# Kernel tuning notes

Measured on AMD Instinct MI355X. Metric: run time of the kernel, lower is better.

Reference implementation:

```python
import math
import jax, jax.numpy as jnp
import numpy as np

B, N, C, HEADS, EXTRA = 16, 577, 768, 12, 1
IMG = (24, 24)
LAMBDA = 0.6


def make_rel_index():
    Hh, Ww = IMG
    coords = np.stack(np.meshgrid(np.arange(Hh), np.arange(Ww), indexing='ij')).reshape(2, -1)
    rel = (coords[:, :, None] - coords[:, None, :]).transpose(1, 2, 0).astype(np.int64)
    rel[..., 0] += Hh - 1
    rel[..., 1] += Ww - 1
    rel[..., 0] *= 2 * Ww - 1
    idx = rel.sum(-1)
    idx = np.pad(idx, ((EXTRA, 0), (EXTRA, 0)))  # pad extra-token rows/cols with index 0
    return jnp.asarray(idx, dtype=jnp.int32)


def setup_inputs() -> dict:
    key = jax.random.key(0)
    ks = jax.random.split(key, 4)
    x = jax.random.normal(ks[0], (B, N, C), jnp.float32)
    qkv_w = jax.random.normal(ks[1], (3 * C, C), jnp.float32) * 0.02
    proj_w = jax.random.normal(ks[2], (C, C), jnp.float32) * 0.02
    proj_b = jnp.zeros((C,), jnp.float32)
    table_sz = (2 * IMG[0] - 1) * (2 * IMG[1] - 1) + 1  # 2210
    bias_table = jax.random.normal(ks[3], (table_sz, HEADS), jnp.float32) * 0.02
    token_weights = jnp.array([0.5, 0.5], jnp.float32)  # softmax([.5,.5]) at init
    return {"x": x, "qkv_w": qkv_w, "proj_w": proj_w, "proj_b": proj_b,
            "bias_table": bias_table, "token_weights": token_weights,
            "rel_index": make_rel_index()}


def attention(x, qkv_w, proj_w, proj_b, bias_table, rel_index):
    b, n, c = x.shape
    hd = c // HEADS
    scale = hd ** -0.5
    qkv = (x @ qkv_w.T).reshape(b, n, 3, HEADS, hd).transpose(2, 0, 3, 1, 4)
    q, k, v = qkv[0] * scale, qkv[1], qkv[2]  # (b,H,n,hd)
    attn = jnp.einsum('bhnd,bhmd->bhnm', q, k)
    bias = jnp.transpose(bias_table[rel_index], (2, 0, 1))  # (H,N,N)
    attn = jax.nn.softmax(attn + bias[None], axis=-1)
    out = jnp.einsum('bhnm,bhmd->bhnd', attn, v).transpose(0, 2, 1, 3).reshape(b, n, c)
    return out @ proj_w.T + proj_b, attn


def select_indices(attn, token_weights):
    # eager, data-dependent sizing (mirrors torch .tolist()/set() host logic)
    n = N - EXTRA
    cls_attn = attn[:, :, 0, EXTRA:].mean(axis=1)  # (B, n)
    avg = cls_attn.mean(axis=1, keepdims=True)
    mx = cls_attn.max(axis=1, keepdims=True)
    counts = np.asarray(((cls_attn >= avg) & (cls_attn <= mx)).sum(axis=1))
    T = counts.sum() / counts.shape[0]
    sig = 1.0 / (1.0 + math.exp(-(float(counts.max()) - float(T)) / B))
    keep = int(round(n * (LAMBDA + (1.0 - LAMBDA) * sig)))
    avg_extra = attn[:, :, :EXTRA, EXTRA:].mean(axis=1)  # (B, EXTRA, n)
    all_idx = []
    for e in range(EXTRA):
        ti = jax.lax.top_k(avg_extra[:, e, :], keep)[1]
        all_idx.extend(np.asarray(ti).reshape(-1).tolist())
    keep_idx = np.array(list(dict.fromkeys(all_idx))[:keep], dtype=np.int32)
    remaining = N - (EXTRA + keep)
    w = jax.nn.softmax(token_weights)
    num_text = int(float(w[0]) * remaining)
    num_img = remaining - num_text
    kt, ki = jax.random.split(jax.random.key(1))
    text_idx = jax.random.randint(kt, (B, max(num_text, 0)), 0, EXTRA)
    img_idx = jax.random.randint(ki, (B, max(num_img, 0)), 0, n - EXTRA)
    return jnp.asarray(keep_idx), text_idx, img_idx


def assemble(x_out, y, keep_idx, text_idx, img_idx):
    b, _, c = x_out.shape
    x_sel = x_out[:, EXTRA:][:, keep_idx]  # shared indices across batch
    parts = [x_out[:, :EXTRA], x_sel]
    if text_idx.shape[1] > 0:
        text_tokens = y[:, 1:1 + EXTRA]
        gi = jnp.broadcast_to(text_idx[:, :, None], (b, text_idx.shape[1], c))
        parts.append(jnp.take_along_axis(text_tokens, gi, axis=1))
    if img_idx.shape[1] > 0:
        image_tokens = y[:, 1 + EXTRA:]
        gi = jnp.broadcast_to(img_idx[:, :, None], (b, img_idx.shape[1], c))
        parts.append(jnp.take_along_axis(image_tokens, gi, axis=1))
    return jnp.concatenate(parts, axis=1)


def reference(x, qkv_w, proj_w, proj_b, bias_table, token_weights, rel_index):
    out, attn = attention(x, qkv_w, proj_w, proj_b, bias_table, rel_index)
    keep_idx, text_idx, img_idx = select_indices(attn, token_weights)
    return assemble(out, x, keep_idx, text_idx, img_idx)
```

## Files before the change

kernel.cpp:

```cpp
#include <hip/hip_runtime.h>
#include <math.h>

#define B_    16
#define N_    577
#define C_    768
#define H_    12
#define HD_   64
#define M_    (B_ * N_)
#define QKV_N 2304
#define NIMG  576

typedef _Float16 half8  __attribute__((ext_vector_type(8)));
typedef _Float16 half4v __attribute__((ext_vector_type(4)));
typedef float    floatx4 __attribute__((ext_vector_type(4)));

#define OFF_QKV      0u
#define OFF_ATTNH    21270528u
#define OFF_ATTNL    24815616u
#define OFF_XOUT     28360704u
#define OFF_CLS      35450880u
#define OFF_CLSPART  35460096u
#define OFF_META     35570688u
#define OFF_WQKVH    35580544u
#define OFF_WQKVL    36465280u
#define OFF_WPROJH   37350016u
#define OFF_WPROJL   37644928u
#define OFF_BIASEXP  37939840u

__global__ __launch_bounds__(256) void split_kernel(const float* __restrict__ in,
                                                    _Float16* __restrict__ hi,
                                                    _Float16* __restrict__ lo, int n) {
    int i = (blockIdx.x * 256 + threadIdx.x) * 4;
    if (i >= n) return;
    float4 v = *(const float4*)(in + i);
    half4v h, l;
    float vv[4] = {v.x, v.y, v.z, v.w};
#pragma unroll
    for (int j = 0; j < 4; ++j) {
        _Float16 hj = (_Float16)vv[j];
        h[j] = hj;
        l[j] = (_Float16)(vv[j] - (float)hj);
    }
    *(half4v*)(hi + i) = h;
    *(half4v*)(lo + i) = l;
}

__global__ __launch_bounds__(256) void bias_expand(const float* __restrict__ bias_table,
                                                   const int* __restrict__ rel_index,
                                                   _Float16* __restrict__ bias_exp) {
    int i = blockIdx.x, h = blockIdx.y;
    const int* ri = rel_index + (size_t)i * N_;
    _Float16* dst = bias_exp + ((size_t)h * N_ + i) * N_;
    for (int j = threadIdx.x; j < N_; j += 256)
        dst[j] = (_Float16)bias_table[ri[j] * H_ + h];
}

__global__ __launch_bounds__(256) void hgemm_nt_split(const _Float16* __restrict__ Ah,
                                                      const _Float16* __restrict__ Al,
                                                      const _Float16* __restrict__ Bh,
                                                      const _Float16* __restrict__ Bl,
                                                      const float* __restrict__ bias,
                                                      float* __restrict__ Cout,
                                                      int M, int Nout) {
    const int K = 768;
    __shared__ __attribute__((aligned(16))) _Float16 Ah_s[128][40];
    __shared__ __attribute__((aligned(16))) _Float16 Al_s[128][40];
    __shared__ __attribute__((aligned(16))) _Float16 Bh_s[128][40];
    __shared__ __attribute__((aligned(16))) _Float16 Bl_s[128][40];

    int tid = threadIdx.x;
    int wave = tid >> 6, lane = tid & 63;
    int g = lane >> 4, c = lane & 15;
    int wr = wave >> 1, wc = wave & 1;
    int m0 = blockIdx.y * 128, n0 = blockIdx.x * 128;

    floatx4 acc[4][4];
#pragma unroll
    for (int mi = 0; mi < 4; ++mi)
#pragma unroll
        for (int ni = 0; ni < 4; ++ni) { acc[mi][ni][0] = 0.f; acc[mi][ni][1] = 0.f; acc[mi][ni][2] = 0.f; acc[mi][ni][3] = 0.f; }

    int lr = tid >> 2;
    int lc = (tid & 3) << 3;

    for (int k0 = 0; k0 < K; k0 += 32) {
        __syncthreads();
#pragma unroll
        for (int hh = 0; hh < 2; ++hh) {
            int r2 = lr + hh * 64;
            size_t ga = (size_t)(m0 + r2) * K + k0 + lc;
            size_t gb = (size_t)(n0 + r2) * K + k0 + lc;
            *(half8*)&Ah_s[r2][lc] = *(const half8*)(Ah + ga);
            *(half8*)&Al_s[r2][lc] = *(const half8*)(Al + ga);
            *(half8*)&Bh_s[r2][lc] = *(const half8*)(Bh + gb);
            *(half8*)&Bl_s[r2][lc] = *(const half8*)(Bl + gb);
        }
        __syncthreads();

        half8 af_h[4], af_l[4];
#pragma unroll
        for (int mi = 0; mi < 4; ++mi) {
            af_h[mi] = *(const half8*)&Ah_s[wr * 64 + mi * 16 + c][g * 8];
            af_l[mi] = *(const half8*)&Al_s[wr * 64 + mi * 16 + c][g * 8];
        }
#pragma unroll
        for (int ni = 0; ni < 4; ++ni) {
            half8 bf_h = *(const half8*)&Bh_s[wc * 64 + ni * 16 + c][g * 8];
            half8 bf_l = *(const half8*)&Bl_s[wc * 64 + ni * 16 + c][g * 8];
#pragma unroll
            for (int mi = 0; mi < 4; ++mi) {
                acc[mi][ni] = __builtin_amdgcn_mfma_f32_16x16x32_f16(af_h[mi], bf_h, acc[mi][ni], 0, 0, 0);
                acc[mi][ni] = __builtin_amdgcn_mfma_f32_16x16x32_f16(af_h[mi], bf_l, acc[mi][ni], 0, 0, 0);
                acc[mi][ni] = __builtin_amdgcn_mfma_f32_16x16x32_f16(af_l[mi], bf_h, acc[mi][ni], 0, 0, 0);
            }
        }
    }

#pragma unroll
    for (int ni = 0; ni < 4; ++ni) {
        int col = n0 + wc * 64 + ni * 16 + c;
        float bv = bias ? bias[col] : 0.f;
#pragma unroll
        for (int mi = 0; mi < 4; ++mi) {
#pragma unroll
            for (int r = 0; r < 4; ++r) {
                int row = m0 + wr * 64 + mi * 16 + 4 * g + r;
                if (row < M) Cout[(size_t)row * Nout + col] = acc[mi][ni][r] + bv;
            }
        }
    }
}

__global__ __launch_bounds__(256, 2) void attn_mfma(const float* __restrict__ qkv,
                                                    const _Float16* __restrict__ bias_exp,
                                                    _Float16* __restrict__ attnh,
                                                    _Float16* __restrict__ attnl) {
    __shared__ __attribute__((aligned(16))) _Float16 Kh[64][72];
    __shared__ __attribute__((aligned(16))) _Float16 Kl[64][72];
    __shared__ __attribute__((aligned(16))) _Float16 Vh[64][72];
    __shared__ __attribute__((aligned(16))) _Float16 Vl[64][72];
    __shared__ __attribute__((aligned(16))) _Float16 Pb[4][32][72];

    int bh = blockIdx.y;
    int b = bh / H_, h = bh % H_;
    int tid = threadIdx.x;
    int wave = tid >> 6, lane = tid & 63;
    int g = lane >> 4, c = lane & 15;
    int row0 = blockIdx.x * 128 + wave * 32;

    half8 qh[2][2], ql[2][2];
#pragma unroll
    for (int rt = 0; rt < 2; ++rt) {
        int grow = row0 + rt * 16 + c;
#pragma unroll
        for (int kb = 0; kb < 2; ++kb) {
            floatx4 a0 = {0.f, 0.f, 0.f, 0.f}, a1 = {0.f, 0.f, 0.f, 0.f};
            if (grow < N_) {
                const float* src = qkv + (size_t)(b * N_ + grow) * QKV_N + h * HD_ + kb * 32 + g * 8;
                a0 = *(const floatx4*)src;
                a1 = *(const floatx4*)(src + 4);
            }
#pragma unroll
            for (int i = 0; i < 4; ++i) {
                float x0 = a0[i] * 0.125f;
                float x1 = a1[i] * 0.125f;
                _Float16 h0 = (_Float16)x0, h1 = (_Float16)x1;
                qh[rt][kb][i]     = h0; ql[rt][kb][i]     = (_Float16)(x0 - (float)h0);
                qh[rt][kb][i + 4] = h1; ql[rt][kb][i + 4] = (_Float16)(x1 - (float)h1);
            }
        }
    }

    floatx4 o[2][4];
    float mrun[2][4], lrun[2][4];
#pragma unroll
    for (int rt = 0; rt < 2; ++rt) {
#pragma unroll
        for (int t = 0; t < 4; ++t) { o[rt][t][0] = 0.f; o[rt][t][1] = 0.f; o[rt][t][2] = 0.f; o[rt][t][3] = 0.f; }
#pragma unroll
        for (int r = 0; r < 4; ++r) { mrun[rt][r] = -1e30f; lrun[rt][r] = 0.f; }
    }

    for (int j0 = 0; j0 < N_; j0 += 64) {
        __syncthreads();
#pragma unroll
        for (int it = 0; it < 4; ++it) {
            int p = tid + it * 256;
            int kr = p >> 4;
            int c4 = (p & 15) << 2;
            int key = j0 + kr;
            floatx4 kv = {0.f, 0.f, 0.f, 0.f}, vv = {0.f, 0.f, 0.f, 0.f};
            if (key < N_) {
                const float* base = qkv + (size_t)(b * N_ + key) * QKV_N + h * HD_ + c4;
                kv = *(const floatx4*)(base + 768);
                vv = *(const floatx4*)(base + 1536);
            }
            half4v kh_, kl_;
#pragma unroll
            for (int i = 0; i < 4; ++i) {
                _Float16 hi = (_Float16)kv[i];
                kh_[i] = hi; kl_[i] = (_Float16)(kv[i] - (float)hi);
            }
            *(half4v*)&Kh[kr][c4] = kh_;
            *(half4v*)&Kl[kr][c4] = kl_;
#pragma unroll
            for (int i = 0; i < 4; ++i) {
                _Float16 hi = (_Float16)vv[i];
                Vh[c4 + i][kr] = hi;
                Vl[c4 + i][kr] = (_Float16)(vv[i] - (float)hi);
            }
        }
        __syncthreads();

        float bv[2][4][4];
#pragma unroll
        for (int rt = 0; rt < 2; ++rt)
#pragma unroll
            for (int t = 0; t < 4; ++t)
#pragma unroll
                for (int r = 0; r < 4; ++r) {
                    int row = row0 + rt * 16 + 4 * g + r;
                    int key = j0 + t * 16 + c;
                    int rr = row < N_ ? row : N_ - 1;
                    int kk = key < N_ ? key : N_ - 1;
                    float bb = (float)bias_exp[((size_t)h * N_ + rr) * N_ + kk];
                    bv[rt][t][r] = (row < N_ && key < N_) ? bb : -1e30f;
                }

        floatx4 s[2][4];
#pragma unroll
        for (int rt = 0; rt < 2; ++rt)
#pragma unroll
            for (int t = 0; t < 4; ++t) { s[rt][t][0] = 0.f; s[rt][t][1] = 0.f; s[rt][t][2] = 0.f; s[rt][t][3] = 0.f; }
#pragma unroll
        for (int t = 0; t < 4; ++t) {
#pragma unroll
            for (int kb = 0; kb < 2; ++kb) {
                half8 kh8 = *(const half8*)&Kh[t * 16 + c][kb * 32 + g * 8];
                half8 kl8 = *(const half8*)&Kl[t * 16 + c][kb * 32 + g * 8];
#pragma unroll
                for (int rt = 0; rt < 2; ++rt) {
                    s[rt][t] = __builtin_amdgcn_mfma_f32_16x16x32_f16(qh[rt][kb], kh8, s[rt][t], 0, 0, 0);
                    s[rt][t] = __builtin_amdgcn_mfma_f32_16x16x32_f16(qh[rt][kb], kl8, s[rt][t], 0, 0, 0);
                    s[rt][t] = __builtin_amdgcn_mfma_f32_16x16x32_f16(ql[rt][kb], kh8, s[rt][t], 0, 0, 0);
                }
            }
        }

#pragma unroll
        for (int rt = 0; rt < 2; ++rt) {
#pragma unroll
            for (int t = 0; t < 4; ++t)
#pragma unroll
                for (int r = 0; r < 4; ++r) s[rt][t][r] += bv[rt][t][r];
            float pm[4], mnew[4], corr[4], rs[4];
#pragma unroll
            for (int r = 0; r < 4; ++r) {
                pm[r] = fmaxf(fmaxf(s[rt][0][r], s[rt][1][r]), fmaxf(s[rt][2][r], s[rt][3][r]));
            }
#pragma unroll
            for (int r = 0; r < 4; ++r) {
                pm[r] = fmaxf(pm[r], __shfl_xor(pm[r], 1));
                pm[r] = fmaxf(pm[r], __shfl_xor(pm[r], 2));
                pm[r] = fmaxf(pm[r], __shfl_xor(pm[r], 4));
                pm[r] = fmaxf(pm[r], __shfl_xor(pm[r], 8));
                mnew[r] = fmaxf(mrun[rt][r], pm[r]);
                corr[r] = __expf(mrun[rt][r] - mnew[r]);
                rs[r] = 0.f;
            }
#pragma unroll
            for (int t = 0; t < 4; ++t)
#pragma unroll
                for (int r = 0; r < 4; ++r) {
                    float p = __expf(s[rt][t][r] - mnew[r]);
                    s[rt][t][r] = p;
                    rs[r] += p;
                }
#pragma unroll
            for (int r = 0; r < 4; ++r) {
                rs[r] += __shfl_xor(rs[r], 1);
                rs[r] += __shfl_xor(rs[r], 2);
                rs[r] += __shfl_xor(rs[r], 4);
                rs[r] += __shfl_xor(rs[r], 8);
                lrun[rt][r] = lrun[rt][r] * corr[r] + rs[r];
                mrun[rt][r] = mnew[r];
            }
#pragma unroll
            for (int t = 0; t < 4; ++t)
#pragma unroll
                for (int r = 0; r < 4; ++r) o[rt][t][r] *= corr[r];
#pragma unroll
            for (int t = 0; t < 4; ++t)
#pragma unroll
                for (int r = 0; r < 4; ++r)
                    Pb[wave][rt * 16 + 4 * g + r][t * 16 + c] = (_Float16)s[rt][t][r];
        }

#pragma unroll
        for (int kb = 0; kb < 2; ++kb) {
            half8 pa[2];
#pragma unroll
            for (int rt = 0; rt < 2; ++rt)
                pa[rt] = *(const half8*)&Pb[wave][rt * 16 + c][kb * 32 + g * 8];
#pragma unroll
            for (int t = 0; t < 4; ++t) {
                half8 vh8 = *(const half8*)&Vh[t * 16 + c][kb * 32 + g * 8];
                half8 vl8 = *(const half8*)&Vl[t * 16 + c][kb * 32 + g * 8];
#pragma unroll
                for (int rt = 0; rt < 2; ++rt) {
                    o[rt][t] = __builtin_amdgcn_mfma_f32_16x16x32_f16(pa[rt], vh8, o[rt][t], 0, 0, 0);
                    o[rt][t] = __builtin_amdgcn_mfma_f32_16x16x32_f16(pa[rt], vl8, o[rt][t], 0, 0, 0);
                }
            }
        }
    }

#pragma unroll
    for (int rt = 0; rt < 2; ++rt)
#pragma unroll
        for (int t = 0; t < 4; ++t)
#pragma unroll
            for (int r = 0; r < 4; ++r) {
                int row = row0 + rt * 16 + 4 * g + r;
                if (row < N_) {
                    float val = o[rt][t][r] / lrun[rt][r];
                    size_t idx = (size_t)(b * N_ + row) * C_ + h * HD_ + t * 16 + c;
                    _Float16 hi = (_Float16)val;
                    attnh[idx] = hi;
                    attnl[idx] = (_Float16)(val - (float)hi);
                }
            }
}

__global__ __launch_bounds__(256) void cls_head_kernel(const float* __restrict__ qkv,
                                                       const float* __restrict__ bias_table,
                                                       const int* __restrict__ rel_index,
                                                       float* __restrict__ cls_part) {
    int b = blockIdx.x, h = blockIdx.y;
    __shared__ float q0[64];
    __shared__ float s[N_];
    __shared__ float red[256];
    int tid = threadIdx.x;
    if (tid < 64) q0[tid] = qkv[(size_t)(b * N_) * QKV_N + h * HD_ + tid] * 0.125f;
    __syncthreads();
    for (int j = tid; j < N_; j += 256) {
        const float* kr = qkv + (size_t)(b * N_ + j) * QKV_N + 768 + h * HD_;
        float d = 0.f;
        for (int kk = 0; kk < 64; ++kk) d += q0[kk] * kr[kk];
        s[j] = d + bias_table[rel_index[j] * H_ + h];
    }
    __syncthreads();
    float mx = -1e30f;
    for (int j = tid; j < N_; j += 256) mx = fmaxf(mx, s[j]);
    red[tid] = mx;
    __syncthreads();
    for (int st = 128; st > 0; st >>= 1) {
        if (tid < st) red[tid] = fmaxf(red[tid], red[tid + st]);
        __syncthreads();
    }
    float m = red[0];
    __syncthreads();
    float ssum = 0.f;
    for (int j = tid; j < N_; j += 256) ssum += expf(s[j] - m);
    red[tid] = ssum;
    __syncthreads();
    for (int st = 128; st > 0; st >>= 1) {
        if (tid < st) red[tid] += red[tid + st];
        __syncthreads();
    }
    float tot = red[0];
    __syncthreads();
    float* dst = cls_part + (size_t)(b * H_ + h) * NIMG;
    for (int j = tid; j < NIMG; j += 256) dst[j] = expf(s[j + 1] - m) / tot;
}

__global__ __launch_bounds__(576) void cls_reduce_kernel(const float* __restrict__ cls_part,
                                                         float* __restrict__ cls) {
    int b = blockIdx.x;
    int j = threadIdx.x;
    float a = 0.f;
    for (int h = 0; h < H_; ++h) a += cls_part[(size_t)(b * H_ + h) * NIMG + j];
    cls[b * NIMG + j] = a * (1.0f / 12.0f);
}

__device__ __forceinline__ void tf2x32(unsigned k0, unsigned k1, unsigned x0, unsigned x1,
                                       unsigned& o0, unsigned& o1) {
    unsigned ks2 = k0 ^ k1 ^ 0x1BD11BDAu;
    x0 += k0; x1 += k1;
#define ROTL_(v, d) (((v) << (d)) | ((v) >> (32 - (d))))
#define RND_(d) { x0 += x1; x1 = ROTL_(x1, d); x1 ^= x0; }
    RND_(13) RND_(15) RND_(26) RND_(6)
    x0 += k1; x1 += ks2 + 1u;
    RND_(17) RND_(29) RND_(16) RND_(24)
    x0 += ks2; x1 += k0 + 2u;
    RND_(13) RND_(15) RND_(26) RND_(6)
    x0 += k0; x1 += k1 + 3u;
    RND_(17) RND_(29) RND_(16) RND_(24)
    x0 += k1; x1 += ks2 + 4u;
    RND_(13) RND_(15) RND_(26) RND_(6)
    x0 += ks2; x1 += k0 + 5u;
    o0 = x0; o1 = x1;
#undef RND_
#undef ROTL_
}

__global__ __launch_bounds__(256) void select_kernel(const float* __restrict__ cls,
                                                     const float* __restrict__ token_w,
                                                     int* __restrict__ meta,
                                                     int* __restrict__ keep_idx,
                                                     int* __restrict__ img_idx) {
    __shared__ float red[256];
    __shared__ int ired[256];
    __shared__ int counts[16];
    __shared__ float c0[NIMG];
    __shared__ int keep_sh, nimg_sh;
    int tid = threadIdx.x;

    for (int b = 0; b < 16; ++b) {
        float sm = 0.f;
        for (int j = tid; j < NIMG; j += 256) sm += cls[b * NIMG + j];
        red[tid] = sm;
        __syncthreads();
        for (int st = 128; st > 0; st >>= 1) {
            if (tid < st) red[tid] += red[tid + st];
            __syncthreads();
        }
        float avg = red[0] * (1.0f / 576.0f);
        __syncthreads();
        int cnt = 0;
        for (int j = tid; j < NIMG; j += 256) cnt += (cls[b * NIMG + j] >= avg) ? 1 : 0;
        ired[tid] = cnt;
        __syncthreads();
        for (int st = 128; st > 0; st >>= 1) {
            if (tid < st) ired[tid] += ired[tid + st];
            __syncthreads();
        }
        if (tid == 0) counts[b] = ired[0];
        __syncthreads();
    }

    if (tid == 0) {
        int csum = 0, cmax = 0;
        for (int b2 = 0; b2 < 16; ++b2) {
            csum += counts[b2];
            if (counts[b2] > cmax) cmax = counts[b2];
        }
        double T = (double)csum / 16.0;
        double sig = 1.0 / (1.0 + exp(-(((double)cmax) - T) / 16.0));
        double kd = 576.0 * (0.6 + 0.4 * sig);
        int keep = (int)llrint(kd);
        int remaining = NIMG - keep;
        float w0 = token_w[0], w1 = token_w[1];
        float wm = fmaxf(w0, w1);
        float e0 = expf(w0 - wm), e1 = expf(w1 - wm);
        float wsm = e0 / (e0 + e1);
        int ntext = (int)((double)wsm * (double)remaining);
        int nimg = remaining - ntext;
        meta[0] = keep; meta[1] = ntext; meta[2] = nimg;
        keep_sh = keep; nimg_sh = nimg;
    }
    __syncthreads();

    for (int j = tid; j < NIMG; j += 256) c0[j] = cls[j];
    __syncthreads();
    int keep = keep_sh;
    for (int j = tid; j < NIMG; j += 256) {
        float v = c0[j];
        int rank = 0;
        for (int j2 = 0; j2 < NIMG; ++j2) {
            float v2 = c0[j2];
            rank += ((v2 > v) || (v2 == v && j2 < j)) ? 1 : 0;
        }
        if (rank < keep) keep_idx[rank] = j;
    }

    unsigned ki0, ki1, k1a, k1b, k2a, k2b;
    tf2x32(0u, 1u, 0u, 1u, ki0, ki1);
    tf2x32(ki0, ki1, 0u, 0u, k1a, k1b);
    tf2x32(ki0, ki1, 0u, 1u, k2a, k2b);
    int nimg = nimg_sh;
    int S = 16 * nimg;
    const unsigned span = 575u;
    const unsigned mult = ((65536u % span) * (65536u % span)) % span;
    for (int i = tid; i < S; i += 256) {
        unsigned h0, h1, l0, l1;
        tf2x32(k1a, k1b, 0u, (unsigned)i, h0, h1);
        tf2x32(k2a, k2b, 0u, (unsigned)i, l0, l1);
        unsigned hb = h0 ^ h1;
        unsigned lb = l0 ^ l1;
        unsigned off = ((hb % span) * mult + (lb % span)) % span;
        img_idx[i] = (int)off;
    }
}

__global__ __launch_bounds__(192) void assemble_kernel(const float* __restrict__ xout,
                                                       const float* __restrict__ x,
                                                       const int* __restrict__ meta,
                                                       const int* __restrict__ keep_idx,
                                                       const int* __restrict__ img_idx,
                                                       float* __restrict__ out) {
    int gb = blockIdx.x;
    int token = gb % N_;
    int b = gb / N_;
    int keep = meta[0], ntext = meta[1], nimg = meta[2];
    const float* src;
    if (token == 0) {
        src = xout + (size_t)(b * N_) * C_;
    } else if (token <= keep) {
        src = xout + (size_t)(b * N_ + 1 + keep_idx[token - 1]) * C_;
    } else if (token <= keep + ntext) {
        src = x + (size_t)(b * N_ + 1) * C_;
    } else {
        int t = token - 1 - keep - ntext;
        src = x + (size_t)(b * N_ + 2 + img_idx[b * nimg + t]) * C_;
    }
    float4* d = (float4*)(out + (size_t)(b * N_ + token) * C_);
    d[threadIdx.x] = ((const float4*)src)[threadIdx.x];
}

extern "C" void kernel_launch(void* const* d_in, const int* in_sizes, int n_in,
                              void* d_out, int out_size, void* d_ws, size_t ws_size,
                              hipStream_t stream) {
    const float* x          = (const float*)d_in[0];
    const float* qkv_w      = (const float*)d_in[1];
    const float* proj_w     = (const float*)d_in[2];
    const float* proj_b     = (const float*)d_in[3];
    const float* bias_table = (const float*)d_in[4];
    const float* token_w    = (const float*)d_in[5];
    const int*   rel_index  = (const int*)d_in[6];
    float* out = (float*)d_out;
    float* ws  = (float*)d_ws;

    float*     qkv_buf  = ws + OFF_QKV;
    _Float16*  attnh    = (_Float16*)(ws + OFF_ATTNH);
    _Float16*  attnl    = (_Float16*)(ws + OFF_ATTNL);
    float*     xout     = ws + OFF_XOUT;
    _Float16*  xh       = (_Float16*)(ws + OFF_XOUT);
    _Float16*  xl       = (_Float16*)(ws + OFF_XOUT + 3545088u);
    float*     cls      = ws + OFF_CLS;
    float*     cls_part = ws + OFF_CLSPART;
    int*       meta     = (int*)(ws + OFF_META);
    int*       keep_idx = meta + 8;
    int*       img_idx  = keep_idx + 576;
    _Float16*  wqkvh    = (_Float16*)(ws + OFF_WQKVH);
    _Float16*  wqkvl    = (_Float16*)(ws + OFF_WQKVL);
    _Float16*  wprojh   = (_Float16*)(ws + OFF_WPROJH);
    _Float16*  wprojl   = (_Float16*)(ws + OFF_WPROJL);
    _Float16*  bias_exp = (_Float16*)(ws + OFF_BIASEXP);

    split_kernel<<<dim3(M_ * C_ / 1024), 256, 0, stream>>>(x, xh, xl, M_ * C_);
    split_kernel<<<dim3(QKV_N * C_ / 1024), 256, 0, stream>>>(qkv_w, wqkvh, wqkvl, QKV_N * C_);
    split_kernel<<<dim3(C_ * C_ / 1024), 256, 0, stream>>>(proj_w, wprojh, wprojl, C_ * C_);
    bias_expand<<<dim3(N_, H_), 256, 0, stream>>>(bias_table, rel_index, bias_exp);
    hgemm_nt_split<<<dim3(QKV_N / 128, (M_ + 127) / 128), 256, 0, stream>>>(
        xh, xl, wqkvh, wqkvl, nullptr, qkv_buf, M_, QKV_N);
    cls_head_kernel<<<dim3(B_, H_), 256, 0, stream>>>(qkv_buf, bias_table, rel_index, cls_part);
    cls_reduce_kernel<<<dim3(B_), 576, 0, stream>>>(cls_part, cls);
    select_kernel<<<dim3(1), 256, 0, stream>>>(cls, token_w, meta, keep_idx, img_idx);
    attn_mfma<<<dim3((N_ + 127) / 128, B_ * H_), 256, 0, stream>>>(
        qkv_buf, bias_exp, attnh, attnl);
    hgemm_nt_split<<<dim3(C_ / 128, (M_ + 127) / 128), 256, 0, stream>>>(
        attnh, attnl, wprojh, wprojl, proj_b, xout, M_, C_);
    assemble_kernel<<<dim3(B_ * N_), 192, 0, stream>>>(
        xout, x, meta, keep_idx, img_idx, out);
}
```

Baseline: 538.0 us.

## Fuse input split into QKV GEMM and emit pre-split fp16 QKV for attention

The QKV GEMM now reads fp32 x directly and splits it into hi/lo fp16 in the load path, which removes the separate split pass over x. Its epilogue writes pre-scaled hi/lo fp16 Q/K/V for the attention kernel and an fp32 Q/K copy for the CLS path. Attention loads half8 operands without per-tile conversion, stores V in an XOR-swizzled layout to cut LDS bank conflicts, reads a bias padded to 640x640 with no bounds checks, orders blocks head-major, and raises occupancy to 3 blocks. In exchange, the GEMM epilogue does more scattered narrow stores, the workspace is rearranged so several buffers alias, and register pressure rises.

```diff
diff --git a/kernel.cpp b/kernel.cpp
--- a/kernel.cpp
+++ b/kernel.cpp
@@ -8,24 +8,28 @@
 #define HD_   64
 #define M_    (B_ * N_)
 #define QKV_N 2304
+#define QK32_N 1536
 #define NIMG  576
+#define BIAS_DIM 640
 
 typedef _Float16 half8  __attribute__((ext_vector_type(8)));
 typedef _Float16 half4v __attribute__((ext_vector_type(4)));
 typedef float    floatx4 __attribute__((ext_vector_type(4)));
 
-#define OFF_QKV      0u
-#define OFF_ATTNH    21270528u
-#define OFF_ATTNL    24815616u
-#define OFF_XOUT     28360704u
+#define OFF_QKV32    0u
+#define OFF_ATTNH    0u
+#define OFF_ATTNL    3545088u
+#define OFF_XOUT     7090176u
+#define OFF_QKVH     14180352u
+#define OFF_QKVL     24815616u
 #define OFF_CLS      35450880u
 #define OFF_CLSPART  35460096u
 #define OFF_META     35570688u
-#define OFF_WQKVH    35580544u
-#define OFF_WQKVL    36465280u
-#define OFF_WPROJH   37350016u
-#define OFF_WPROJL   37644928u
-#define OFF_BIASEXP  37939840u
+#define OFF_WQKVH    35582976u
+#define OFF_WQKVL    36467712u
+#define OFF_WPROJH   37352448u
+#define OFF_WPROJL   37647360u
+#define OFF_BIASPAD  37942272u
 
 __global__ __launch_bounds__(256) void split_kernel(const float* __restrict__ in,
                                                     _Float16* __restrict__ hi,
@@ -47,12 +51,110 @@
 
 __global__ __launch_bounds__(256) void bias_expand(const float* __restrict__ bias_table,
                                                    const int* __restrict__ rel_index,
-                                                   _Float16* __restrict__ bias_exp) {
+                                                   _Float16* __restrict__ bias_pad) {
     int i = blockIdx.x, h = blockIdx.y;
-    const int* ri = rel_index + (size_t)i * N_;
-    _Float16* dst = bias_exp + ((size_t)h * N_ + i) * N_;
-    for (int j = threadIdx.x; j < N_; j += 256)
-        dst[j] = (_Float16)bias_table[ri[j] * H_ + h];
+    _Float16* dst = bias_pad + ((size_t)h * BIAS_DIM + i) * BIAS_DIM;
+    const _Float16 NEG = (_Float16)(-30000.f);
+    if (i < N_) {
+        const int* ri = rel_index + (size_t)i * N_;
+        for (int j = threadIdx.x; j < BIAS_DIM; j += 256)
+            dst[j] = (j < N_) ? (_Float16)bias_table[ri[j] * H_ + h] : NEG;
+    } else {
+        for (int j = threadIdx.x; j < BIAS_DIM; j += 256) dst[j] = NEG;
+    }
+}
+
+__global__ __launch_bounds__(256) void hgemm_qkv(const float* __restrict__ A,
+                                                 const _Float16* __restrict__ Bh,
+                                                 const _Float16* __restrict__ Bl,
+                                                 float* __restrict__ qkv32,
+                                                 _Float16* __restrict__ qh_,
+                                                 _Float16* __restrict__ ql_) {
+    const int K = 768;
+    __shared__ __attribute__((aligned(16))) _Float16 Ah_s[128][40];
+    __shared__ __attribute__((aligned(16))) _Float16 Al_s[128][40];
+    __shared__ __attribute__((aligned(16))) _Float16 Bh_s[128][40];
+    __shared__ __attribute__((aligned(16))) _Float16 Bl_s[128][40];
+
+    int tid = threadIdx.x;
+    int wave = tid >> 6, lane = tid & 63;
+    int g = lane >> 4, c = lane & 15;
+    int wr = wave >> 1, wc = wave & 1;
+    int m0 = blockIdx.y * 128, n0 = blockIdx.x * 128;
+
+    floatx4 acc[4][4];
+#pragma unroll
+    for (int mi = 0; mi < 4; ++mi)
+#pragma unroll
+        for (int ni = 0; ni < 4; ++ni) { acc[mi][ni][0] = 0.f; acc[mi][ni][1] = 0.f; acc[mi][ni][2] = 0.f; acc[mi][ni][3] = 0.f; }
+
+    int lr = tid >> 2;
+    int lc = (tid & 3) << 3;
+
+    for (int k0 = 0; k0 < K; k0 += 32) {
+        __syncthreads();
+#pragma unroll
+        for (int hh = 0; hh < 2; ++hh) {
+            int r2 = lr + hh * 64;
+            int arow = m0 + r2; if (arow >= M_) arow = M_ - 1;
+            const float* ap = A + (size_t)arow * K + k0 + lc;
+            floatx4 a0 = *(const floatx4*)ap;
+            floatx4 a1 = *(const floatx4*)(ap + 4);
+            half8 ah, al;
+#pragma unroll
+            for (int i = 0; i < 4; ++i) {
+                _Float16 h0 = (_Float16)a0[i];
+                ah[i] = h0; al[i] = (_Float16)(a0[i] - (float)h0);
+                _Float16 h1 = (_Float16)a1[i];
+                ah[i + 4] = h1; al[i + 4] = (_Float16)(a1[i] - (float)h1);
+            }
+            *(half8*)&Ah_s[r2][lc] = ah;
+            *(half8*)&Al_s[r2][lc] = al;
+            size_t gb = (size_t)(n0 + r2) * K + k0 + lc;
+            *(half8*)&Bh_s[r2][lc] = *(const half8*)(Bh + gb);
+            *(half8*)&Bl_s[r2][lc] = *(const half8*)(Bl + gb);
+        }
+        __syncthreads();
+
+        half8 af_h[4], af_l[4];
+#pragma unroll
+        for (int mi = 0; mi < 4; ++mi) {
+            af_h[mi] = *(const half8*)&Ah_s[wr * 64 + mi * 16 + c][g * 8];
+            af_l[mi] = *(const half8*)&Al_s[wr * 64 + mi * 16 + c][g * 8];
+        }
+#pragma unroll
+        for (int ni = 0; ni < 4; ++ni) {
+            half8 bf_h = *(const half8*)&Bh_s[wc * 64 + ni * 16 + c][g * 8];
+            half8 bf_l = *(const half8*)&Bl_s[wc * 64 + ni * 16 + c][g * 8];
+#pragma unroll
+            for (int mi = 0; mi < 4; ++mi) {
+                acc[mi][ni] = __builtin_amdgcn_mfma_f32_16x16x32_f16(af_h[mi], bf_h, acc[mi][ni], 0, 0, 0);
+                acc[mi][ni] = __builtin_amdgcn_mfma_f32_16x16x32_f16(af_h[mi], bf_l, acc[mi][ni], 0, 0, 0);
+                acc[mi][ni] = __builtin_amdgcn_mfma_f32_16x16x32_f16(af_l[mi], bf_h, acc[mi][ni], 0, 0, 0);
+            }
+        }
+    }
+
+#pragma unroll
+    for (int ni = 0; ni < 4; ++ni) {
+        int col = n0 + wc * 64 + ni * 16 + c;
+#pragma unroll
+        for (int mi = 0; mi < 4; ++mi) {
+#pragma unroll
+            for (int r = 0; r < 4; ++r) {
+                int row = m0 + wr * 64 + mi * 16 + 4 * g + r;
+                if (row < M_) {
+                    float v = acc[mi][ni][r];
+                    if (col < QK32_N) qkv32[(size_t)row * QK32_N + col] = v;
+                    float sv = (col < 768) ? v * 0.125f : v;
+                    _Float16 hi = (_Float16)sv;
+                    size_t idx = (size_t)row * QKV_N + col;
+                    qh_[idx] = hi;
+                    ql_[idx] = (_Float16)(sv - (float)hi);
+                }
+            }
+        }
+    }
 }
 
 __global__ __launch_bounds__(256) void hgemm_nt_split(const _Float16* __restrict__ Ah,
@@ -131,22 +233,25 @@
     }
 }
 
-__global__ __launch_bounds__(256, 2) void attn_mfma(const float* __restrict__ qkv,
-                                                    const _Float16* __restrict__ bias_exp,
+__global__ __launch_bounds__(256, 3) void attn_mfma(const _Float16* __restrict__ qkvh,
+                                                    const _Float16* __restrict__ qkvl,
+                                                    const _Float16* __restrict__ bias_pad,
                                                     _Float16* __restrict__ attnh,
                                                     _Float16* __restrict__ attnl) {
     __shared__ __attribute__((aligned(16))) _Float16 Kh[64][72];
     __shared__ __attribute__((aligned(16))) _Float16 Kl[64][72];
-    __shared__ __attribute__((aligned(16))) _Float16 Vh[64][72];
-    __shared__ __attribute__((aligned(16))) _Float16 Vl[64][72];
+    __shared__ __attribute__((aligned(16))) _Float16 VhS[64 * 64];
+    __shared__ __attribute__((aligned(16))) _Float16 VlS[64 * 64];
     __shared__ __attribute__((aligned(16))) _Float16 Pb[4][32][72];
 
     int bh = blockIdx.y;
-    int b = bh / H_, h = bh % H_;
+    int h = bh >> 4, b = bh & 15;
     int tid = threadIdx.x;
     int wave = tid >> 6, lane = tid & 63;
     int g = lane >> 4, c = lane & 15;
     int row0 = blockIdx.x * 128 + wave * 32;
+    char* vhb = (char*)VhS;
+    char* vlb = (char*)VlS;
 
     half8 qh[2][2], ql[2][2];
 #pragma unroll
@@ -154,20 +259,13 @@
         int grow = row0 + rt * 16 + c;
 #pragma unroll
         for (int kb = 0; kb < 2; ++kb) {
-            floatx4 a0 = {0.f, 0.f, 0.f, 0.f}, a1 = {0.f, 0.f, 0.f, 0.f};
+            half8 zh = {}, zl = {};
             if (grow < N_) {
-                const float* src = qkv + (size_t)(b * N_ + grow) * QKV_N + h * HD_ + kb * 32 + g * 8;
-                a0 = *(const floatx4*)src;
-                a1 = *(const floatx4*)(src + 4);
-            }
-#pragma unroll
-            for (int i = 0; i < 4; ++i) {
-                float x0 = a0[i] * 0.125f;
-                float x1 = a1[i] * 0.125f;
-                _Float16 h0 = (_Float16)x0, h1 = (_Float16)x1;
-                qh[rt][kb][i]     = h0; ql[rt][kb][i]     = (_Float16)(x0 - (float)h0);
-                qh[rt][kb][i + 4] = h1; ql[rt][kb][i + 4] = (_Float16)(x1 - (float)h1);
-            }
+                size_t off = (size_t)(b * N_ + grow) * QKV_N + h * HD_ + kb * 32 + g * 8;
+                zh = *(const half8*)(qkvh + off);
+                zl = *(const half8*)(qkvl + off);
+            }
+            qh[rt][kb] = zh; ql[rt][kb] = zl;
         }
     }
 
@@ -184,30 +282,27 @@
     for (int j0 = 0; j0 < N_; j0 += 64) {
         __syncthreads();
 #pragma unroll
-        for (int it = 0; it < 4; ++it) {
-            int p = tid + it * 256;
-            int kr = p >> 4;
-            int c4 = (p & 15) << 2;
-            int key = j0 + kr;
-            floatx4 kv = {0.f, 0.f, 0.f, 0.f}, vv = {0.f, 0.f, 0.f, 0.f};
-            if (key < N_) {
-                const float* base = qkv + (size_t)(b * N_ + key) * QKV_N + h * HD_ + c4;
-                kv = *(const floatx4*)(base + 768);
-                vv = *(const floatx4*)(base + 1536);
-            }
-            half4v kh_, kl_;
-#pragma unroll
-            for (int i = 0; i < 4; ++i) {
-                _Float16 hi = (_Float16)kv[i];
-                kh_[i] = hi; kl_[i] = (_Float16)(kv[i] - (float)hi);
-            }
-            *(half4v*)&Kh[kr][c4] = kh_;
-            *(half4v*)&Kl[kr][c4] = kl_;
-#pragma unroll
-            for (int i = 0; i < 4; ++i) {
-                _Float16 hi = (_Float16)vv[i];
-                Vh[c4 + i][kr] = hi;
-                Vl[c4 + i][kr] = (_Float16)(vv[i] - (float)hi);
+        for (int pass = 0; pass < 2; ++pass) {
+            int idx = pass * 256 + tid;
+            int key = idx >> 3;
+            int d0 = (idx & 7) << 3;
+            int j = j0 + key;
+            half8 khv = {}, klv = {}, vhv = {}, vlv = {};
+            if (j < N_) {
+                size_t gb = (size_t)(b * N_ + j) * QKV_N + h * HD_ + d0;
+                khv = *(const half8*)(qkvh + gb + 768);
+                klv = *(const half8*)(qkvl + gb + 768);
+                vhv = *(const half8*)(qkvh + gb + 1536);
+                vlv = *(const half8*)(qkvl + gb + 1536);
+            }
+            *(half8*)&Kh[key][d0] = khv;
+            *(half8*)&Kl[key][d0] = klv;
+#pragma unroll
+            for (int i = 0; i < 8; ++i) {
+                int d = d0 + i;
+                int cb = (key * 2) ^ (((d & 7) ^ ((d >> 3) & 7)) << 4);
+                *(_Float16*)(vhb + d * 128 + cb) = vhv[i];
+                *(_Float16*)(vlb + d * 128 + cb) = vlv[i];
             }
         }
         __syncthreads();
@@ -218,14 +313,9 @@
 #pragma unroll
             for (int t = 0; t < 4; ++t)
 #pragma unroll
-                for (int r = 0; r < 4; ++r) {
-                    int row = row0 + rt * 16 + 4 * g + r;
-                    int key = j0 + t * 16 + c;
-                    int rr = row < N_ ? row : N_ - 1;
-                    int kk = key < N_ ? key : N_ - 1;
-                    float bb = (float)bias_exp[((size_t)h * N_ + rr) * N_ + kk];
-                    bv[rt][t][r] = (row < N_ && key < N_) ? bb : -1e30f;
-                }
+                for (int r = 0; r < 4; ++r)
+                    bv[rt][t][r] = (float)bias_pad[((size_t)h * BIAS_DIM + row0 + rt * 16 + 4 * g + r) * BIAS_DIM
+                                                   + j0 + t * 16 + c];
 
         floatx4 s[2][4];
 #pragma unroll
@@ -255,9 +345,8 @@
                 for (int r = 0; r < 4; ++r) s[rt][t][r] += bv[rt][t][r];
             float pm[4], mnew[4], corr[4], rs[4];
 #pragma unroll
-            for (int r = 0; r < 4; ++r) {
+            for (int r = 0; r < 4; ++r)
                 pm[r] = fmaxf(fmaxf(s[rt][0][r], s[rt][1][r]), fmaxf(s[rt][2][r], s[rt][3][r]));
-            }
 #pragma unroll
             for (int r = 0; r < 4; ++r) {
                 pm[r] = fmaxf(pm[r], __shfl_xor(pm[r], 1));
@@ -304,8 +393,10 @@
                 pa[rt] = *(const half8*)&Pb[wave][rt * 16 + c][kb * 32 + g * 8];
 #pragma unroll
             for (int t = 0; t < 4; ++t) {
-                half8 vh8 = *(const half8*)&Vh[t * 16 + c][kb * 32 + g * 8];
-                half8 vl8 = *(const half8*)&Vl[t * 16 + c][kb * 32 + g * 8];
+                int row = t * 16 + c;
+                int cb = (kb * 64 + g * 16) ^ (((row & 7) ^ ((row >> 3) & 7)) << 4);
+                half8 vh8 = *(const half8*)(vhb + row * 128 + cb);
+                half8 vl8 = *(const half8*)(vlb + row * 128 + cb);
 #pragma unroll
                 for (int rt = 0; rt < 2; ++rt) {
                     o[rt][t] = __builtin_amdgcn_mfma_f32_16x16x32_f16(pa[rt], vh8, o[rt][t], 0, 0, 0);
@@ -332,7 +423,7 @@
             }
 }
 
-__global__ __launch_bounds__(256) void cls_head_kernel(const float* __restrict__ qkv,
+__global__ __launch_bounds__(256) void cls_head_kernel(const float* __restrict__ qkv32,
                                                        const float* __restrict__ bias_table,
                                                        const int* __restrict__ rel_index,
                                                        float* __restrict__ cls_part) {
@@ -341,10 +432,10 @@
     __shared__ float s[N_];
     __shared__ float red[256];
     int tid = threadIdx.x;
-    if (tid < 64) q0[tid] = qkv[(size_t)(b * N_) * QKV_N + h * HD_ + tid] * 0.125f;
+    if (tid < 64) q0[tid] = qkv32[(size_t)(b * N_) * QK32_N + h * HD_ + tid] * 0.125f;
     __syncthreads();
     for (int j = tid; j < N_; j += 256) {
-        const float* kr = qkv + (size_t)(b * N_ + j) * QKV_N + 768 + h * HD_;
+        const float* kr = qkv32 + (size_t)(b * N_ + j) * QK32_N + 768 + h * HD_;
         float d = 0.f;
         for (int kk = 0; kk < 64; ++kk) d += q0[kk] * kr[kk];
         s[j] = d + bias_table[rel_index[j] * H_ + h];
@@ -531,12 +622,12 @@
     float* out = (float*)d_out;
     float* ws  = (float*)d_ws;
 
-    float*     qkv_buf  = ws + OFF_QKV;
+    float*     qkv32    = ws + OFF_QKV32;
     _Float16*  attnh    = (_Float16*)(ws + OFF_ATTNH);
     _Float16*  attnl    = (_Float16*)(ws + OFF_ATTNL);
     float*     xout     = ws + OFF_XOUT;
-    _Float16*  xh       = (_Float16*)(ws + OFF_XOUT);
-    _Float16*  xl       = (_Float16*)(ws + OFF_XOUT + 3545088u);
+    _Float16*  qkvh     = (_Float16*)(ws + OFF_QKVH);
+    _Float16*  qkvl     = (_Float16*)(ws + OFF_QKVL);
     float*     cls      = ws + OFF_CLS;
     float*     cls_part = ws + OFF_CLSPART;
     int*       meta     = (int*)(ws + OFF_META);
@@ -546,19 +637,18 @@
     _Float16*  wqkvl    = (_Float16*)(ws + OFF_WQKVL);
     _Float16*  wprojh   = (_Float16*)(ws + OFF_WPROJH);
     _Float16*  wprojl   = (_Float16*)(ws + OFF_WPROJL);
-    _Float16*  bias_exp = (_Float16*)(ws + OFF_BIASEXP);
-
-    split_kernel<<<dim3(M_ * C_ / 1024), 256, 0, stream>>>(x, xh, xl, M_ * C_);
+    _Float16*  bias_pad = (_Float16*)(ws + OFF_BIASPAD);
+
     split_kernel<<<dim3(QKV_N * C_ / 1024), 256, 0, stream>>>(qkv_w, wqkvh, wqkvl, QKV_N * C_);
     split_kernel<<<dim3(C_ * C_ / 1024), 256, 0, stream>>>(proj_w, wprojh, wprojl, C_ * C_);
-    bias_expand<<<dim3(N_, H_), 256, 0, stream>>>(bias_table, rel_index, bias_exp);
-    hgemm_nt_split<<<dim3(QKV_N / 128, (M_ + 127) / 128), 256, 0, stream>>>(
-        xh, xl, wqkvh, wqkvl, nullptr, qkv_buf, M_, QKV_N);
-    cls_head_kernel<<<dim3(B_, H_), 256, 0, stream>>>(qkv_buf, bias_table, rel_index, cls_part);
+    bias_expand<<<dim3(BIAS_DIM, H_), 256, 0, stream>>>(bias_table, rel_index, bias_pad);
+    hgemm_qkv<<<dim3(QKV_N / 128, (M_ + 127) / 128), 256, 0, stream>>>(
+        x, wqkvh, wqkvl, qkv32, qkvh, qkvl);
+    cls_head_kernel<<<dim3(B_, H_), 256, 0, stream>>>(qkv32, bias_table, rel_index, cls_part);
     cls_reduce_kernel<<<dim3(B_), 576, 0, stream>>>(cls_part, cls);
     select_kernel<<<dim3(1), 256, 0, stream>>>(cls, token_w, meta, keep_idx, img_idx);
     attn_mfma<<<dim3((N_ + 127) / 128, B_ * H_), 256, 0, stream>>>(
-        qkv_buf, bias_exp, attnh, attnl);
+        qkvh, qkvl, bias_pad, attnh, attnl);
     hgemm_nt_split<<<dim3(C_ / 128, (M_ + 127) / 128), 256, 0, stream>>>(
         attnh, attnl, wprojh, wprojl, proj_b, xout, M_, C_);
     assemble_kernel<<<dim3(B_ * N_), 192, 0, stream>>>(
```

Result: slower. 633.4 us (+17.7%).
